# Performance work log

Measured on AMD Instinct MI355X. Metric: run time of the kernel, lower is better.

Reference implementation:

```python
import jax, jax.numpy as jnp
import numpy as np

H = 2048      # hidden_size
I = 8192      # dense intermediate_size
MI = 1024     # moe_intermediate_size
E = 8         # num_local_experts
K = 2         # num_experts_per_tok
B, S = 2, 1024
EPS = 1e-6
ROOT = H ** (-0.5)


def _rms(x, w=None, eps=EPS):
    # fp32 RMSNorm matching _Gemma4CPURMSNorm; w=None -> no-scale variant
    ms = jnp.mean(x * x, axis=-1, keepdims=True) + eps
    y = x * jax.lax.rsqrt(ms)
    return y * w if w is not None else y


def _gelu_tanh(x):
    # gelu_pytorch_tanh == tanh-approximate gelu
    return jax.nn.gelu(x, approximate=True)


def setup_inputs() -> dict:
    key = jax.random.key(0)
    ks = jax.random.split(key, 10)
    s = 0.02
    return {
        "hidden_states": jax.random.normal(ks[0], (B, S, H), jnp.float32),
        # RMSNorm scales (init ones, as in nn.Parameter(torch.ones(dim)))
        "rn_pre1": jnp.ones((H,), jnp.float32),
        "rn_pre2": jnp.ones((H,), jnp.float32),
        "rn_post1": jnp.ones((H,), jnp.float32),
        "rn_post2": jnp.ones((H,), jnp.float32),
        "rn_post": jnp.ones((H,), jnp.float32),
        # dense GLU MLP weights, stored (in, out)
        "w_gate": jax.random.normal(ks[1], (H, I), jnp.float32) * s,
        "w_up":   jax.random.normal(ks[2], (H, I), jnp.float32) * s,
        "w_down": jax.random.normal(ks[3], (I, H), jnp.float32) * s,
        # router
        "router_w": jax.random.normal(ks[4], (H, E), jnp.float32) * s,
        "router_scale": jnp.ones((H,), jnp.float32),
        "per_expert_scale": jnp.ones((E,), jnp.float32),
        # per-expert GLU weights, stacked over experts
        "we_gate": jax.random.normal(ks[5], (E, H, MI), jnp.float32) * s,
        "we_up":   jax.random.normal(ks[6], (E, H, MI), jnp.float32) * s,
        "we_down": jax.random.normal(ks[7], (E, MI, H), jnp.float32) * s,
    }


def reference(hidden_states, rn_pre1, rn_pre2, rn_post1, rn_post2, rn_post,
              w_gate, w_up, w_down, router_w, router_scale, per_expert_scale,
              we_gate, we_up, we_down):
    b, s, h = hidden_states.shape
    T = b * s

    # --- dense branch ---
    dense_in = _rms(hidden_states, rn_pre1)                      # (B,S,H)
    dense_out = (_gelu_tanh(dense_in @ w_gate) * (dense_in @ w_up)) @ w_down
    dense_out = _rms(dense_out, rn_post1)                        # (B,S,H)

    # --- router (takes the raw residual, applies its own no-scale RMSNorm) ---
    x = hidden_states.reshape(T, h)
    xr = _rms(x) * router_scale * ROOT                           # (T,H)
    router_logits = xr @ router_w                                # (T,E)
    probs = jax.nn.softmax(router_logits, axis=-1)
    top_w, top_i = jax.lax.top_k(probs, K)                       # (T,K)
    top_w = top_w / jnp.sum(top_w, axis=-1, keepdims=True)
    top_w = top_w * per_expert_scale[top_i]
    aff = jnp.zeros((T, E), x.dtype).at[jnp.arange(T)[:, None], top_i].set(top_w)

    # --- MoE experts (compute all experts, combine with sparse affinities) ---
    moe_in = _rms(hidden_states, rn_pre2).reshape(T, h)          # (T,H)
    g = jnp.einsum('th,ehm->tem', moe_in, we_gate)               # (T,E,MI)
    u = jnp.einsum('th,ehm->tem', moe_in, we_up)
    eo = jnp.einsum('tem,emh->teh', _gelu_tanh(g) * u, we_down)  # (T,E,H)
    moe_out = jnp.einsum('te,teh->th', aff, eo).reshape(b, s, h)
    moe_out = _rms(moe_out, rn_post2)

    return _rms(dense_out + moe_out, rn_post)
```

## Files before the change

### kernel.cpp

```cpp
#include <hip/hip_runtime.h>
#include <stdint.h>

#define TOK 2048
#define HD  2048
#define ID  8192
#define MID 1024
#define NE  8

typedef __attribute__((ext_vector_type(8))) short s16x8;
typedef __attribute__((ext_vector_type(4))) short s16x4;
typedef __attribute__((ext_vector_type(4))) float f32x4;

constexpr float EPSF  = 1e-6f;
constexpr float ROOTF = 0.02209708691207961f;

#define MFMA(a, b, c) __builtin_amdgcn_mfma_f32_16x16x32_bf16(a, b, c, 0, 0, 0)

__device__ __forceinline__ short f2bf(float f) {
  union { float f; uint32_t u; } v; v.f = f;
  uint32_t r = v.u + 0x7fffu + ((v.u >> 16) & 1u);
  return (short)(r >> 16);
}

__device__ __forceinline__ float gelu_tanh(float x) {
  float x3 = x * x * x;
  float u = 0.7978845608028654f * (x + 0.044715f * x3);
  return 0.5f * x * (1.0f + tanhf(u));
}

__global__ __launch_bounds__(256) void k_rms_router(
    const float* __restrict__ x, const float* __restrict__ rnp1,
    const float* __restrict__ rnp2, const float* __restrict__ rsc,
    const float* __restrict__ rw, const float* __restrict__ pes,
    short* __restrict__ rms1, short* __restrict__ rms2,
    int* __restrict__ cnt, int* __restrict__ tokl,
    float* __restrict__ wgtl, int* __restrict__ slotl) {
  const int t = blockIdx.x, tid = threadIdx.x;
  const size_t base = (size_t)t * HD;
  f32x4 v[2];
  float ss = 0.f;
#pragma unroll
  for (int i = 0; i < 2; ++i) {
    v[i] = *(const f32x4*)(x + base + tid * 4 + i * 1024);
#pragma unroll
    for (int j = 0; j < 4; ++j) ss += v[i][j] * v[i][j];
  }
  __shared__ float sr[4];
  __shared__ float sl[32];
#pragma unroll
  for (int off = 32; off; off >>= 1) ss += __shfl_down(ss, off, 64);
  if ((tid & 63) == 0) sr[tid >> 6] = ss;
  __syncthreads();
  const float inv = rsqrtf((sr[0] + sr[1] + sr[2] + sr[3]) * (1.0f / HD) + EPSF);
  float p[8] = {0, 0, 0, 0, 0, 0, 0, 0};
#pragma unroll
  for (int i = 0; i < 2; ++i) {
    const int h = tid * 4 + i * 1024;
    f32x4 w1 = *(const f32x4*)(rnp1 + h);
    f32x4 w2 = *(const f32x4*)(rnp2 + h);
    f32x4 sc = *(const f32x4*)(rsc + h);
    s16x4 o1, o2;
#pragma unroll
    for (int j = 0; j < 4; ++j) {
      float xn = v[i][j] * inv;
      o1[j] = f2bf(xn * w1[j]);
      o2[j] = f2bf(xn * w2[j]);
      float xq = xn * sc[j] * ROOTF;
      const float* rr = rw + (size_t)(h + j) * NE;
      f32x4 ra = *(const f32x4*)rr;
      f32x4 rb = *(const f32x4*)(rr + 4);
      p[0] += xq * ra[0]; p[1] += xq * ra[1]; p[2] += xq * ra[2]; p[3] += xq * ra[3];
      p[4] += xq * rb[0]; p[5] += xq * rb[1]; p[6] += xq * rb[2]; p[7] += xq * rb[3];
    }
    *(s16x4*)(rms1 + base + h) = o1;
    *(s16x4*)(rms2 + base + h) = o2;
  }
#pragma unroll
  for (int e = 0; e < 8; ++e)
#pragma unroll
    for (int off = 32; off; off >>= 1) p[e] += __shfl_down(p[e], off, 64);
  if ((tid & 63) == 0) {
#pragma unroll
    for (int e = 0; e < 8; ++e) sl[(tid >> 6) * 8 + e] = p[e];
  }
  __syncthreads();
  if (tid == 0) {
    float l[8];
#pragma unroll
    for (int e = 0; e < 8; ++e) l[e] = sl[e] + sl[8 + e] + sl[16 + e] + sl[24 + e];
    int i1 = 0;
#pragma unroll
    for (int e = 1; e < 8; ++e) if (l[e] > l[i1]) i1 = e;
    int i2 = (i1 == 0) ? 1 : 0;
#pragma unroll
    for (int e = 0; e < 8; ++e) if (e != i1 && l[e] > l[i2]) i2 = e;
    float p2 = expf(l[i2] - l[i1]);
    float s = 1.0f + p2;
    float w1 = (1.0f / s) * pes[i1];
    float w2 = (p2 / s) * pes[i2];
    int q1 = atomicAdd(&cnt[i1], 1);
    tokl[i1 * TOK + q1] = t; wgtl[i1 * TOK + q1] = w1; slotl[i1 * TOK + q1] = 0;
    int q2 = atomicAdd(&cnt[i2], 1);
    tokl[i2 * TOK + q2] = t; wgtl[i2 * TOK + q2] = w2; slotl[i2 * TOK + q2] = 1;
  }
}

__global__ __launch_bounds__(256) void k_transpose(
    const float* __restrict__ in, short* __restrict__ out, int R, int C) {
  __shared__ float tile[64 * 65];
  const int tid = threadIdx.x;
  const int c0 = blockIdx.x * 64, r0 = blockIdx.y * 64;
  const size_t bo = (size_t)blockIdx.z * R * C;
#pragma unroll
  for (int i = 0; i < 4; ++i) {
    int idx = tid + 256 * i;
    int r = idx >> 4, c4 = idx & 15;
    f32x4 f = *(const f32x4*)(in + bo + (size_t)(r0 + r) * C + c0 + c4 * 4);
#pragma unroll
    for (int j = 0; j < 4; ++j) tile[(c4 * 4 + j) * 65 + r] = f[j];
  }
  __syncthreads();
#pragma unroll
  for (int i = 0; i < 2; ++i) {
    int ch = tid + 256 * i;
    int c = ch >> 3, rs = ch & 7;
    s16x8 o;
#pragma unroll
    for (int q = 0; q < 8; ++q) o[q] = f2bf(tile[c * 65 + rs * 8 + q]);
    *(s16x8*)(out + bo + (size_t)(c0 + c) * R + r0 + rs * 8) = o;
  }
}

__global__ __launch_bounds__(256) void k_dense_gateup(
    const short* __restrict__ wgT, const short* __restrict__ wuT,
    const short* __restrict__ xin,
    short* __restrict__ act) {
  __shared__ short sW[128 * 32];
  __shared__ short sX[128 * 32];
  const int tid = threadIdx.x;
  const int n0 = blockIdx.x * 64, t0 = blockIdx.y * 128;
  const int lane = tid & 63, wave = tid >> 6;
  const int ln15 = lane & 15, k8 = (lane >> 4) * 8;
  const int nsub = (wave & 1) * 32, tsub = (wave >> 1) * 64;
  const int srow = tid >> 2, skc = (tid & 3) * 8;
  const short* gW0 = wgT + (size_t)(n0 + srow) * HD + skc;
  const short* gW1 = wuT + (size_t)(n0 + srow) * HD + skc;
  const short* gX0 = xin + (size_t)(t0 + srow) * HD + skc;
  const short* gX1 = xin + (size_t)(t0 + 64 + srow) * HD + skc;
  short* dW0 = sW + tid * 8;
  short* dW1 = sW + (tid + 256) * 8;
  short* dX0 = sX + tid * 8;
  short* dX1 = sX + (tid + 256) * 8;
  f32x4 accg[2][4], accu[2][4];
#pragma unroll
  for (int m = 0; m < 2; ++m)
#pragma unroll
    for (int n = 0; n < 4; ++n) { accg[m][n] = (f32x4)0.f; accu[m][n] = (f32x4)0.f; }
  for (int kt = 0; kt < HD / 32; ++kt) {
    const int ko = kt * 32;
    s16x8 w0 = *(const s16x8*)(gW0 + ko);
    s16x8 w1 = *(const s16x8*)(gW1 + ko);
    s16x8 x0 = *(const s16x8*)(gX0 + ko);
    s16x8 x1 = *(const s16x8*)(gX1 + ko);
    __syncthreads();
    *(s16x8*)dW0 = w0; *(s16x8*)dW1 = w1;
    *(s16x8*)dX0 = x0; *(s16x8*)dX1 = x1;
    __syncthreads();
    s16x8 ag[2], au[2], bx[4];
#pragma unroll
    for (int m = 0; m < 2; ++m) {
      ag[m] = *(const s16x8*)(sW + (nsub + m * 16 + ln15) * 32 + k8);
      au[m] = *(const s16x8*)(sW + (64 + nsub + m * 16 + ln15) * 32 + k8);
    }
#pragma unroll
    for (int n = 0; n < 4; ++n)
      bx[n] = *(const s16x8*)(sX + (tsub + n * 16 + ln15) * 32 + k8);
#pragma unroll
    for (int m = 0; m < 2; ++m)
#pragma unroll
      for (int n = 0; n < 4; ++n) {
        accg[m][n] = MFMA(ag[m], bx[n], accg[m][n]);
        accu[m][n] = MFMA(au[m], bx[n], accu[m][n]);
      }
  }
#pragma unroll
  for (int m = 0; m < 2; ++m)
#pragma unroll
    for (int n = 0; n < 4; ++n) {
      const int t = t0 + tsub + n * 16 + ln15;
      const int ib = n0 + nsub + m * 16 + (lane >> 4) * 4;
      s16x4 o;
#pragma unroll
      for (int r = 0; r < 4; ++r)
        o[r] = f2bf(gelu_tanh(accg[m][n][r]) * accu[m][n][r]);
      *(s16x4*)(act + (size_t)t * ID + ib) = o;
    }
}

__global__ __launch_bounds__(256) void k_dense_down(
    const short* __restrict__ wdT,
    const short* __restrict__ act,
    float* __restrict__ dh) {
  __shared__ short sW[128 * 32];
  __shared__ short sX[64 * 32];
  const int tid = threadIdx.x;
  const int n0 = blockIdx.x * 128, t0 = blockIdx.y * 64;
  const int lane = tid & 63, wave = tid >> 6;
  const int ln15 = lane & 15, k8 = (lane >> 4) * 8;
  const int srow = tid >> 2, skc = (tid & 3) * 8;
  const short* gW0 = wdT + (size_t)(n0 + srow) * ID + skc;
  const short* gW1 = wdT + (size_t)(n0 + 64 + srow) * ID + skc;
  const short* gX0 = act + (size_t)(t0 + srow) * ID + skc;
  short* dW0 = sW + tid * 8;
  short* dW1 = sW + (tid + 256) * 8;
  short* dX0 = sX + tid * 8;
  f32x4 acc[2][4];
#pragma unroll
  for (int m = 0; m < 2; ++m)
#pragma unroll
    for (int n = 0; n < 4; ++n) acc[m][n] = (f32x4)0.f;
  for (int kt = 0; kt < ID / 32; ++kt) {
    const int ko = kt * 32;
    s16x8 w0 = *(const s16x8*)(gW0 + ko);
    s16x8 w1 = *(const s16x8*)(gW1 + ko);
    s16x8 x0 = *(const s16x8*)(gX0 + ko);
    __syncthreads();
    *(s16x8*)dW0 = w0; *(s16x8*)dW1 = w1; *(s16x8*)dX0 = x0;
    __syncthreads();
    s16x8 a[2], b[4];
#pragma unroll
    for (int m = 0; m < 2; ++m)
      a[m] = *(const s16x8*)(sW + (wave * 32 + m * 16 + ln15) * 32 + k8);
#pragma unroll
    for (int n = 0; n < 4; ++n)
      b[n] = *(const s16x8*)(sX + (n * 16 + ln15) * 32 + k8);
#pragma unroll
    for (int m = 0; m < 2; ++m)
#pragma unroll
      for (int n = 0; n < 4; ++n) acc[m][n] = MFMA(a[m], b[n], acc[m][n]);
  }
#pragma unroll
  for (int n = 0; n < 4; ++n) {
    const int t = t0 + n * 16 + ln15;
#pragma unroll
    for (int m = 0; m < 2; ++m) {
      const int h = n0 + wave * 32 + m * 16 + (lane >> 4) * 4;
      *(f32x4*)(dh + (size_t)t * HD + h) = acc[m][n];
    }
  }
}

__global__ __launch_bounds__(256) void k_exp_gateup(
    const short* __restrict__ wegT, const short* __restrict__ weuT,
    const short* __restrict__ rms2,
    const int* __restrict__ cnt, const int* __restrict__ tokl,
    short* __restrict__ acte) {
  const int e = blockIdx.z;
  const int cn = cnt[e];
  const int t0 = blockIdx.y * 128;
  if (t0 >= cn) return;
  const int n0 = blockIdx.x * 64;
  __shared__ short sW[128 * 32];
  __shared__ short sX[128 * 32];
  const int tid = threadIdx.x;
  const int lane = tid & 63, wave = tid >> 6;
  const int ln15 = lane & 15, k8 = (lane >> 4) * 8;
  const int nsub = (wave & 1) * 32, tsub = (wave >> 1) * 64;
  const int srow = tid >> 2, skc = (tid & 3) * 8;
  const int* tl = tokl + e * TOK;
  int r0 = t0 + srow, r1 = t0 + 64 + srow;
  int tk0 = tl[r0 < cn ? r0 : cn - 1];
  int tk1 = tl[r1 < cn ? r1 : cn - 1];
  const short* gW0 = wegT + (size_t)e * MID * HD + (size_t)(n0 + srow) * HD + skc;
  const short* gW1 = weuT + (size_t)e * MID * HD + (size_t)(n0 + srow) * HD + skc;
  const short* gX0 = rms2 + (size_t)tk0 * HD + skc;
  const short* gX1 = rms2 + (size_t)tk1 * HD + skc;
  short* dW0 = sW + tid * 8;
  short* dW1 = sW + (tid + 256) * 8;
  short* dX0 = sX + tid * 8;
  short* dX1 = sX + (tid + 256) * 8;
  f32x4 accg[2][4], accu[2][4];
#pragma unroll
  for (int m = 0; m < 2; ++m)
#pragma unroll
    for (int n = 0; n < 4; ++n) { accg[m][n] = (f32x4)0.f; accu[m][n] = (f32x4)0.f; }
  for (int kt = 0; kt < HD / 32; ++kt) {
    const int ko = kt * 32;
    s16x8 w0 = *(const s16x8*)(gW0 + ko);
    s16x8 w1 = *(const s16x8*)(gW1 + ko);
    s16x8 x0 = *(const s16x8*)(gX0 + ko);
    s16x8 x1 = *(const s16x8*)(gX1 + ko);
    __syncthreads();
    *(s16x8*)dW0 = w0; *(s16x8*)dW1 = w1;
    *(s16x8*)dX0 = x0; *(s16x8*)dX1 = x1;
    __syncthreads();
    s16x8 ag[2], au[2], bx[4];
#pragma unroll
    for (int m = 0; m < 2; ++m) {
      ag[m] = *(const s16x8*)(sW + (nsub + m * 16 + ln15) * 32 + k8);
      au[m] = *(const s16x8*)(sW + (64 + nsub + m * 16 + ln15) * 32 + k8);
    }
#pragma unroll
    for (int n = 0; n < 4; ++n)
      bx[n] = *(const s16x8*)(sX + (tsub + n * 16 + ln15) * 32 + k8);
#pragma unroll
    for (int m = 0; m < 2; ++m)
#pragma unroll
      for (int n = 0; n < 4; ++n) {
        accg[m][n] = MFMA(ag[m], bx[n], accg[m][n]);
        accu[m][n] = MFMA(au[m], bx[n], accu[m][n]);
      }
  }
#pragma unroll
  for (int m = 0; m < 2; ++m)
#pragma unroll
    for (int n = 0; n < 4; ++n) {
      const int r = t0 + tsub + n * 16 + ln15;
      if (r < cn) {
        const int ib = n0 + nsub + m * 16 + (lane >> 4) * 4;
        s16x4 o;
#pragma unroll
        for (int q = 0; q < 4; ++q)
          o[q] = f2bf(gelu_tanh(accg[m][n][q]) * accu[m][n][q]);
        *(s16x4*)(acte + (size_t)e * TOK * MID + (size_t)r * MID + ib) = o;
      }
    }
}

__global__ __launch_bounds__(256) void k_exp_down(
    const short* __restrict__ wedT,
    const short* __restrict__ acte,
    const int* __restrict__ cnt, const int* __restrict__ tokl,
    const float* __restrict__ wgtl, const int* __restrict__ slotl,
    float* __restrict__ moep) {
  const int e = blockIdx.z;
  const int cn = cnt[e];
  const int t0 = blockIdx.y * 64;
  if (t0 >= cn) return;
  const int n0 = blockIdx.x * 128;
  __shared__ short sW[128 * 32];
  __shared__ short sX[64 * 32];
  const int tid = threadIdx.x;
  const int lane = tid & 63, wave = tid >> 6;
  const int ln15 = lane & 15, k8 = (lane >> 4) * 8;
  const int srow = tid >> 2, skc = (tid & 3) * 8;
  const short* wb = wedT + (size_t)e * HD * MID;
  const short* gW0 = wb + (size_t)(n0 + srow) * MID + skc;
  const short* gW1 = wb + (size_t)(n0 + 64 + srow) * MID + skc;
  const short* gX0 = acte + (size_t)e * TOK * MID + (size_t)(t0 + srow) * MID + skc;
  short* dW0 = sW + tid * 8;
  short* dW1 = sW + (tid + 256) * 8;
  short* dX0 = sX + tid * 8;
  f32x4 acc[2][4];
#pragma unroll
  for (int m = 0; m < 2; ++m)
#pragma unroll
    for (int n = 0; n < 4; ++n) acc[m][n] = (f32x4)0.f;
  for (int kt = 0; kt < MID / 32; ++kt) {
    const int ko = kt * 32;
    s16x8 w0 = *(const s16x8*)(gW0 + ko);
    s16x8 w1 = *(const s16x8*)(gW1 + ko);
    s16x8 x0 = *(const s16x8*)(gX0 + ko);
    __syncthreads();
    *(s16x8*)dW0 = w0; *(s16x8*)dW1 = w1; *(s16x8*)dX0 = x0;
    __syncthreads();
    s16x8 a[2], b[4];
#pragma unroll
    for (int m = 0; m < 2; ++m)
      a[m] = *(const s16x8*)(sW + (wave * 32 + m * 16 + ln15) * 32 + k8);
#pragma unroll
    for (int n = 0; n < 4; ++n)
      b[n] = *(const s16x8*)(sX + (n * 16 + ln15) * 32 + k8);
#pragma unroll
    for (int m = 0; m < 2; ++m)
#pragma unroll
      for (int n = 0; n < 4; ++n) acc[m][n] = MFMA(a[m], b[n], acc[m][n]);
  }
#pragma unroll
  for (int n = 0; n < 4; ++n) {
    const int r = t0 + n * 16 + ln15;
    if (r < cn) {
      const int tk = tokl[e * TOK + r];
      const float wf = wgtl[e * TOK + r];
      const int sl = slotl[e * TOK + r];
      float* dst = moep + (size_t)sl * TOK * HD + (size_t)tk * HD;
#pragma unroll
      for (int m = 0; m < 2; ++m) {
        const int h = n0 + wave * 32 + m * 16 + (lane >> 4) * 4;
        f32x4 v = acc[m][n] * wf;
        *(f32x4*)(dst + h) = v;
      }
    }
  }
}

__global__ __launch_bounds__(256) void k_final(
    const float* __restrict__ dh, const float* __restrict__ moep,
    const float* __restrict__ rno1, const float* __restrict__ rno2,
    const float* __restrict__ rnof, float* __restrict__ out) {
  const int t = blockIdx.x, tid = threadIdx.x;
  const size_t base = (size_t)t * HD;
  f32x4 dv[2], mv[2];
  float ssd = 0.f, ssm = 0.f;
#pragma unroll
  for (int i = 0; i < 2; ++i) {
    const int h = tid * 4 + i * 1024;
    dv[i] = *(const f32x4*)(dh + base + h);
    f32x4 a = *(const f32x4*)(moep + base + h);
    f32x4 b = *(const f32x4*)(moep + (size_t)TOK * HD + base + h);
    mv[i] = a + b;
#pragma unroll
    for (int j = 0; j < 4; ++j) { ssd += dv[i][j] * dv[i][j]; ssm += mv[i][j] * mv[i][j]; }
  }
  __shared__ float sr[8];
#pragma unroll
  for (int off = 32; off; off >>= 1) {
    ssd += __shfl_down(ssd, off, 64);
    ssm += __shfl_down(ssm, off, 64);
  }
  if ((tid & 63) == 0) { sr[tid >> 6] = ssd; sr[4 + (tid >> 6)] = ssm; }
  __syncthreads();
  const float invd = rsqrtf((sr[0] + sr[1] + sr[2] + sr[3]) * (1.0f / HD) + EPSF);
  const float invm = rsqrtf((sr[4] + sr[5] + sr[6] + sr[7]) * (1.0f / HD) + EPSF);
  f32x4 y[2];
  float ssy = 0.f;
#pragma unroll
  for (int i = 0; i < 2; ++i) {
    const int h = tid * 4 + i * 1024;
    f32x4 w1 = *(const f32x4*)(rno1 + h);
    f32x4 w2 = *(const f32x4*)(rno2 + h);
#pragma unroll
    for (int j = 0; j < 4; ++j) {
      y[i][j] = dv[i][j] * invd * w1[j] + mv[i][j] * invm * w2[j];
      ssy += y[i][j] * y[i][j];
    }
  }
  __syncthreads();
#pragma unroll
  for (int off = 32; off; off >>= 1) ssy += __shfl_down(ssy, off, 64);
  if ((tid & 63) == 0) sr[tid >> 6] = ssy;
  __syncthreads();
  const float invy = rsqrtf((sr[0] + sr[1] + sr[2] + sr[3]) * (1.0f / HD) + EPSF);
#pragma unroll
  for (int i = 0; i < 2; ++i) {
    const int h = tid * 4 + i * 1024;
    f32x4 w = *(const f32x4*)(rnof + h);
    f32x4 o;
#pragma unroll
    for (int j = 0; j < 4; ++j) o[j] = y[i][j] * invy * w[j];
    *(f32x4*)(out + base + h) = o;
  }
}

extern "C" void kernel_launch(void* const* d_in, const int* in_sizes, int n_in,
                              void* d_out, int out_size, void* d_ws, size_t ws_size,
                              hipStream_t stream) {
  (void)in_sizes; (void)n_in; (void)out_size;
  const float* x    = (const float*)d_in[0];
  const float* rnp1 = (const float*)d_in[1];
  const float* rnp2 = (const float*)d_in[2];
  const float* rno1 = (const float*)d_in[3];
  const float* rno2 = (const float*)d_in[4];
  const float* rnof = (const float*)d_in[5];
  const float* wg   = (const float*)d_in[6];
  const float* wu   = (const float*)d_in[7];
  const float* wd   = (const float*)d_in[8];
  const float* rw   = (const float*)d_in[9];
  const float* rsc  = (const float*)d_in[10];
  const float* pes  = (const float*)d_in[11];
  const float* weg  = (const float*)d_in[12];
  const float* weu  = (const float*)d_in[13];
  const float* wed  = (const float*)d_in[14];
  float* out = (float*)d_out;

  char* ws = (char*)d_ws;
  size_t off = 0;
  auto alloc = [&](size_t bytes) -> void* {
    void* p = ws + off;
    off += (bytes + 255) & ~(size_t)255;
    return p;
  };
  const size_t IH  = (size_t)ID * HD;
  const size_t EMH = (size_t)NE * MID * HD;
  short* wgT   = (short*)alloc(IH * 2);
  short* wuT   = (short*)alloc(IH * 2);
  short* wdT   = (short*)alloc(IH * 2);
  short* wegT  = (short*)alloc(EMH * 2);
  short* weuT  = (short*)alloc(EMH * 2);
  short* wedT  = (short*)alloc(EMH * 2);
  short* rms1  = (short*)alloc((size_t)TOK * HD * 2);
  short* rms2  = (short*)alloc((size_t)TOK * HD * 2);
  short* actb  = (short*)alloc((size_t)TOK * ID * 2);
  short* acte  = (short*)alloc((size_t)NE * TOK * MID * 2);
  float* dhb   = (float*)alloc((size_t)TOK * HD * 4);
  float* moep  = (float*)alloc((size_t)2 * TOK * HD * 4);
  int*   cnt   = (int*)alloc(NE * 4);
  int*   tokl  = (int*)alloc((size_t)NE * TOK * 4);
  float* wgtl  = (float*)alloc((size_t)NE * TOK * 4);
  int*   slotl = (int*)alloc((size_t)NE * TOK * 4);
  if (off > ws_size) return;

  hipMemsetAsync(cnt, 0, NE * 4, stream);
  k_rms_router<<<TOK, 256, 0, stream>>>(x, rnp1, rnp2, rsc, rw, pes,
                                        rms1, rms2, cnt, tokl, wgtl, slotl);
  k_transpose<<<dim3(ID / 64, HD / 64, 1), 256, 0, stream>>>(wg, wgT, HD, ID);
  k_transpose<<<dim3(ID / 64, HD / 64, 1), 256, 0, stream>>>(wu, wuT, HD, ID);
  k_transpose<<<dim3(HD / 64, ID / 64, 1), 256, 0, stream>>>(wd, wdT, ID, HD);
  k_transpose<<<dim3(MID / 64, HD / 64, NE), 256, 0, stream>>>(weg, wegT, HD, MID);
  k_transpose<<<dim3(MID / 64, HD / 64, NE), 256, 0, stream>>>(weu, weuT, HD, MID);
  k_transpose<<<dim3(HD / 64, MID / 64, NE), 256, 0, stream>>>(wed, wedT, MID, HD);
  k_dense_gateup<<<dim3(ID / 64, TOK / 128), 256, 0, stream>>>(wgT, wuT, rms1, actb);
  k_dense_down<<<dim3(HD / 128, TOK / 64), 256, 0, stream>>>(wdT, actb, dhb);
  k_exp_gateup<<<dim3(MID / 64, TOK / 128, NE), 256, 0, stream>>>(wegT, weuT, rms2,
                                                                  cnt, tokl, acte);
  k_exp_down<<<dim3(HD / 128, TOK / 64, NE), 256, 0, stream>>>(wedT, acte, cnt, tokl,
                                                               wgtl, slotl, moep);
  k_final<<<TOK, 256, 0, stream>>>(dhb, moep, rno1, rno2, rnof, out);
}
```

Measured before the change: 664.4 us.

## Use direct global-to-LDS loads and enlarge down-projection tiles to 128x128

Replaces the register-staged global loads and LDS stores in all four GEMM kernels with direct global_load_lds 16-byte transfers, which cuts VGPR traffic and instruction count in the staging path. The dense and expert down-projection kernels also grow their token tile from 64 to 128 and use a 2x2 wave layout with 4x4 MFMA fragments each, which raises data reuse per LDS load and halves the number of blocks. In exchange, each wave holds more accumulator registers and the grids are smaller, which may lower occupancy. Staging is still single-buffered with two barriers per k-step, so the async loads do not overlap with compute.

```diff
diff --git a/kernel.cpp b/kernel.cpp
--- a/kernel.cpp
+++ b/kernel.cpp
@@ -15,6 +15,12 @@
 constexpr float ROOTF = 0.02209708691207961f;
 
 #define MFMA(a, b, c) __builtin_amdgcn_mfma_f32_16x16x32_bf16(a, b, c, 0, 0, 0)
+
+__device__ __forceinline__ void gload16(const void* g, void* l) {
+  __builtin_amdgcn_global_load_lds(
+      (const __attribute__((address_space(1))) void*)g,
+      (__attribute__((address_space(3))) void*)l, 16, 0, 0);
+}
 
 __device__ __forceinline__ short f2bf(float f) {
   union { float f; uint32_t u; } v; v.f = f;
@@ -147,10 +153,8 @@
   const short* gW1 = wuT + (size_t)(n0 + srow) * HD + skc;
   const short* gX0 = xin + (size_t)(t0 + srow) * HD + skc;
   const short* gX1 = xin + (size_t)(t0 + 64 + srow) * HD + skc;
-  short* dW0 = sW + tid * 8;
-  short* dW1 = sW + (tid + 256) * 8;
-  short* dX0 = sX + tid * 8;
-  short* dX1 = sX + (tid + 256) * 8;
+  char* lW = (char*)sW + wave * 1024;
+  char* lX = (char*)sX + wave * 1024;
   f32x4 accg[2][4], accu[2][4];
 #pragma unroll
   for (int m = 0; m < 2; ++m)
@@ -158,13 +162,11 @@
     for (int n = 0; n < 4; ++n) { accg[m][n] = (f32x4)0.f; accu[m][n] = (f32x4)0.f; }
   for (int kt = 0; kt < HD / 32; ++kt) {
     const int ko = kt * 32;
-    s16x8 w0 = *(const s16x8*)(gW0 + ko);
-    s16x8 w1 = *(const s16x8*)(gW1 + ko);
-    s16x8 x0 = *(const s16x8*)(gX0 + ko);
-    s16x8 x1 = *(const s16x8*)(gX1 + ko);
-    __syncthreads();
-    *(s16x8*)dW0 = w0; *(s16x8*)dW1 = w1;
-    *(s16x8*)dX0 = x0; *(s16x8*)dX1 = x1;
+    __syncthreads();
+    gload16(gW0 + ko, lW);
+    gload16(gW1 + ko, lW + 4096);
+    gload16(gX0 + ko, lX);
+    gload16(gX1 + ko, lX + 4096);
     __syncthreads();
     s16x8 ag[2], au[2], bx[4];
 #pragma unroll
@@ -202,49 +204,50 @@
     const short* __restrict__ act,
     float* __restrict__ dh) {
   __shared__ short sW[128 * 32];
-  __shared__ short sX[64 * 32];
+  __shared__ short sX[128 * 32];
   const int tid = threadIdx.x;
-  const int n0 = blockIdx.x * 128, t0 = blockIdx.y * 64;
+  const int n0 = blockIdx.x * 128, t0 = blockIdx.y * 128;
   const int lane = tid & 63, wave = tid >> 6;
+  const int wr = wave >> 1, wc = wave & 1;
   const int ln15 = lane & 15, k8 = (lane >> 4) * 8;
   const int srow = tid >> 2, skc = (tid & 3) * 8;
   const short* gW0 = wdT + (size_t)(n0 + srow) * ID + skc;
   const short* gW1 = wdT + (size_t)(n0 + 64 + srow) * ID + skc;
   const short* gX0 = act + (size_t)(t0 + srow) * ID + skc;
-  short* dW0 = sW + tid * 8;
-  short* dW1 = sW + (tid + 256) * 8;
-  short* dX0 = sX + tid * 8;
-  f32x4 acc[2][4];
-#pragma unroll
-  for (int m = 0; m < 2; ++m)
+  const short* gX1 = act + (size_t)(t0 + 64 + srow) * ID + skc;
+  char* lW = (char*)sW + wave * 1024;
+  char* lX = (char*)sX + wave * 1024;
+  f32x4 acc[4][4];
+#pragma unroll
+  for (int m = 0; m < 4; ++m)
 #pragma unroll
     for (int n = 0; n < 4; ++n) acc[m][n] = (f32x4)0.f;
   for (int kt = 0; kt < ID / 32; ++kt) {
     const int ko = kt * 32;
-    s16x8 w0 = *(const s16x8*)(gW0 + ko);
-    s16x8 w1 = *(const s16x8*)(gW1 + ko);
-    s16x8 x0 = *(const s16x8*)(gX0 + ko);
-    __syncthreads();
-    *(s16x8*)dW0 = w0; *(s16x8*)dW1 = w1; *(s16x8*)dX0 = x0;
-    __syncthreads();
-    s16x8 a[2], b[4];
-#pragma unroll
-    for (int m = 0; m < 2; ++m)
-      a[m] = *(const s16x8*)(sW + (wave * 32 + m * 16 + ln15) * 32 + k8);
+    __syncthreads();
+    gload16(gW0 + ko, lW);
+    gload16(gW1 + ko, lW + 4096);
+    gload16(gX0 + ko, lX);
+    gload16(gX1 + ko, lX + 4096);
+    __syncthreads();
+    s16x8 a[4], b[4];
+#pragma unroll
+    for (int m = 0; m < 4; ++m)
+      a[m] = *(const s16x8*)(sW + (wr * 64 + m * 16 + ln15) * 32 + k8);
 #pragma unroll
     for (int n = 0; n < 4; ++n)
-      b[n] = *(const s16x8*)(sX + (n * 16 + ln15) * 32 + k8);
-#pragma unroll
-    for (int m = 0; m < 2; ++m)
+      b[n] = *(const s16x8*)(sX + (wc * 64 + n * 16 + ln15) * 32 + k8);
+#pragma unroll
+    for (int m = 0; m < 4; ++m)
 #pragma unroll
       for (int n = 0; n < 4; ++n) acc[m][n] = MFMA(a[m], b[n], acc[m][n]);
   }
 #pragma unroll
   for (int n = 0; n < 4; ++n) {
-    const int t = t0 + n * 16 + ln15;
-#pragma unroll
-    for (int m = 0; m < 2; ++m) {
-      const int h = n0 + wave * 32 + m * 16 + (lane >> 4) * 4;
+    const int t = t0 + wc * 64 + n * 16 + ln15;
+#pragma unroll
+    for (int m = 0; m < 4; ++m) {
+      const int h = n0 + wr * 64 + m * 16 + (lane >> 4) * 4;
       *(f32x4*)(dh + (size_t)t * HD + h) = acc[m][n];
     }
   }
@@ -275,10 +278,8 @@
   const short* gW1 = weuT + (size_t)e * MID * HD + (size_t)(n0 + srow) * HD + skc;
   const short* gX0 = rms2 + (size_t)tk0 * HD + skc;
   const short* gX1 = rms2 + (size_t)tk1 * HD + skc;
-  short* dW0 = sW + tid * 8;
-  short* dW1 = sW + (tid + 256) * 8;
-  short* dX0 = sX + tid * 8;
-  short* dX1 = sX + (tid + 256) * 8;
+  char* lW = (char*)sW + wave * 1024;
+  char* lX = (char*)sX + wave * 1024;
   f32x4 accg[2][4], accu[2][4];
 #pragma unroll
   for (int m = 0; m < 2; ++m)
@@ -286,13 +287,11 @@
     for (int n = 0; n < 4; ++n) { accg[m][n] = (f32x4)0.f; accu[m][n] = (f32x4)0.f; }
   for (int kt = 0; kt < HD / 32; ++kt) {
     const int ko = kt * 32;
-    s16x8 w0 = *(const s16x8*)(gW0 + ko);
-    s16x8 w1 = *(const s16x8*)(gW1 + ko);
-    s16x8 x0 = *(const s16x8*)(gX0 + ko);
-    s16x8 x1 = *(const s16x8*)(gX1 + ko);
-    __syncthreads();
-    *(s16x8*)dW0 = w0; *(s16x8*)dW1 = w1;
-    *(s16x8*)dX0 = x0; *(s16x8*)dX1 = x1;
+    __syncthreads();
+    gload16(gW0 + ko, lW);
+    gload16(gW1 + ko, lW + 4096);
+    gload16(gX0 + ko, lX);
+    gload16(gX1 + ko, lX + 4096);
     __syncthreads();
     s16x8 ag[2], au[2], bx[4];
 #pragma unroll
@@ -335,58 +334,60 @@
     float* __restrict__ moep) {
   const int e = blockIdx.z;
   const int cn = cnt[e];
-  const int t0 = blockIdx.y * 64;
+  const int t0 = blockIdx.y * 128;
   if (t0 >= cn) return;
   const int n0 = blockIdx.x * 128;
   __shared__ short sW[128 * 32];
-  __shared__ short sX[64 * 32];
+  __shared__ short sX[128 * 32];
   const int tid = threadIdx.x;
   const int lane = tid & 63, wave = tid >> 6;
+  const int wr = wave >> 1, wc = wave & 1;
   const int ln15 = lane & 15, k8 = (lane >> 4) * 8;
   const int srow = tid >> 2, skc = (tid & 3) * 8;
   const short* wb = wedT + (size_t)e * HD * MID;
   const short* gW0 = wb + (size_t)(n0 + srow) * MID + skc;
   const short* gW1 = wb + (size_t)(n0 + 64 + srow) * MID + skc;
-  const short* gX0 = acte + (size_t)e * TOK * MID + (size_t)(t0 + srow) * MID + skc;
-  short* dW0 = sW + tid * 8;
-  short* dW1 = sW + (tid + 256) * 8;
-  short* dX0 = sX + tid * 8;
-  f32x4 acc[2][4];
-#pragma unroll
-  for (int m = 0; m < 2; ++m)
+  const short* ab = acte + (size_t)e * TOK * MID;
+  const short* gX0 = ab + (size_t)(t0 + srow) * MID + skc;
+  const short* gX1 = ab + (size_t)(t0 + 64 + srow) * MID + skc;
+  char* lW = (char*)sW + wave * 1024;
+  char* lX = (char*)sX + wave * 1024;
+  f32x4 acc[4][4];
+#pragma unroll
+  for (int m = 0; m < 4; ++m)
 #pragma unroll
     for (int n = 0; n < 4; ++n) acc[m][n] = (f32x4)0.f;
   for (int kt = 0; kt < MID / 32; ++kt) {
     const int ko = kt * 32;
-    s16x8 w0 = *(const s16x8*)(gW0 + ko);
-    s16x8 w1 = *(const s16x8*)(gW1 + ko);
-    s16x8 x0 = *(const s16x8*)(gX0 + ko);
-    __syncthreads();
-    *(s16x8*)dW0 = w0; *(s16x8*)dW1 = w1; *(s16x8*)dX0 = x0;
-    __syncthreads();
-    s16x8 a[2], b[4];
-#pragma unroll
-    for (int m = 0; m < 2; ++m)
-      a[m] = *(const s16x8*)(sW + (wave * 32 + m * 16 + ln15) * 32 + k8);
+    __syncthreads();
+    gload16(gW0 + ko, lW);
+    gload16(gW1 + ko, lW + 4096);
+    gload16(gX0 + ko, lX);
+    gload16(gX1 + ko, lX + 4096);
+    __syncthreads();
+    s16x8 a[4], b[4];
+#pragma unroll
+    for (int m = 0; m < 4; ++m)
+      a[m] = *(const s16x8*)(sW + (wr * 64 + m * 16 + ln15) * 32 + k8);
 #pragma unroll
     for (int n = 0; n < 4; ++n)
-      b[n] = *(const s16x8*)(sX + (n * 16 + ln15) * 32 + k8);
-#pragma unroll
-    for (int m = 0; m < 2; ++m)
+      b[n] = *(const s16x8*)(sX + (wc * 64 + n * 16 + ln15) * 32 + k8);
+#pragma unroll
+    for (int m = 0; m < 4; ++m)
 #pragma unroll
       for (int n = 0; n < 4; ++n) acc[m][n] = MFMA(a[m], b[n], acc[m][n]);
   }
 #pragma unroll
   for (int n = 0; n < 4; ++n) {
-    const int r = t0 + n * 16 + ln15;
+    const int r = t0 + wc * 64 + n * 16 + ln15;
     if (r < cn) {
       const int tk = tokl[e * TOK + r];
       const float wf = wgtl[e * TOK + r];
       const int sl = slotl[e * TOK + r];
       float* dst = moep + (size_t)sl * TOK * HD + (size_t)tk * HD;
 #pragma unroll
-      for (int m = 0; m < 2; ++m) {
-        const int h = n0 + wave * 32 + m * 16 + (lane >> 4) * 4;
+      for (int m = 0; m < 4; ++m) {
+        const int h = n0 + wr * 64 + m * 16 + (lane >> 4) * 4;
         f32x4 v = acc[m][n] * wf;
         *(f32x4*)(dst + h) = v;
       }
@@ -510,10 +511,10 @@
   k_transpose<<<dim3(MID / 64, HD / 64, NE), 256, 0, stream>>>(weu, weuT, HD, MID);
   k_transpose<<<dim3(HD / 64, MID / 64, NE), 256, 0, stream>>>(wed, wedT, MID, HD);
   k_dense_gateup<<<dim3(ID / 64, TOK / 128), 256, 0, stream>>>(wgT, wuT, rms1, actb);
-  k_dense_down<<<dim3(HD / 128, TOK / 64), 256, 0, stream>>>(wdT, actb, dhb);
+  k_dense_down<<<dim3(HD / 128, TOK / 128), 256, 0, stream>>>(wdT, actb, dhb);
   k_exp_gateup<<<dim3(MID / 64, TOK / 128, NE), 256, 0, stream>>>(wegT, weuT, rms2,
                                                                   cnt, tokl, acte);
-  k_exp_down<<<dim3(HD / 128, TOK / 64, NE), 256, 0, stream>>>(wedT, acte, cnt, tokl,
-                                                               wgtl, slotl, moep);
+  k_exp_down<<<dim3(HD / 128, TOK / 128, NE), 256, 0, stream>>>(wedT, acte, cnt, tokl,
+                                                                wgtl, slotl, moep);
   k_final<<<TOK, 256, 0, stream>>>(dhb, moep, rno1, rno2, rnof, out);
 }
```

Result: slower. 685.5 us (+3.2%).
